# Kernel optimization log

Measured on AMD Instinct MI355X. Metric: run time of the kernel, lower is better.

The kernel has to match this reference:

```python
import jax, jax.numpy as jnp
import numpy as np

D = 32   # embedding/memory dimension
H = 2    # attention heads
DH = D // H
N_TABLE = 1_000_000
NB = 100_000      # batch nodes per type
E = 2_000_000     # edges per edge type
NE_TOT = 4_000_000
F = 32            # raw edge feature dim


def time_enc(t, w, b):
    # TimeEncode: cos(t * w + b), t: [N] -> [N, D]
    return jnp.cos(t[:, None] * w[None, :] + b[None, :])


def edge_attention_agg(h_src, h_dst, ei, ef, te, mask, Wk, Wq, Wv, n_dst):
    """One HGT-style masked multi-head attention aggregation for a single edge type.
    ei: [2, E] (src, dst local indices); ef/te: [E, D]; mask: [E] bool.
    Returns [n_dst, D] aggregated messages (segment-softmax over incoming edges)."""
    src, dst = ei[0], ei[1]
    e = src.shape[0]
    hs = h_src[src]                                   # [E, D] gather
    k = (hs @ Wk).reshape(e, H, DH)
    q = (h_dst[dst] @ Wq).reshape(e, H, DH)
    v = ((hs + ef + te) @ Wv).reshape(e, H, DH)
    s = jnp.sum(q * k, axis=-1) / jnp.sqrt(jnp.asarray(DH, h_src.dtype))  # [E, H]
    s = jnp.where(mask[:, None], s, jnp.asarray(-1e9, s.dtype))
    smax = jax.ops.segment_max(s, dst, num_segments=n_dst)                # [n_dst, H]
    p = jnp.where(mask[:, None], jnp.exp(s - smax[dst]), 0.0)
    den = jax.ops.segment_sum(p, dst, num_segments=n_dst) + 1e-9
    w = p / den[dst]                                                      # [E, H]
    return jax.ops.segment_sum((w[..., None] * v).reshape(e, D), dst, num_segments=n_dst)


def reference(memory_author, memory_paper, edge_feature,
              node_x_author, node_x_paper, ts_author, ts_paper,
              ei_writes, rel_t_writes, eidx_writes, mask_writes,
              ei_rev, rel_t_rev, eidx_rev, mask_rev,
              time_w, time_b,
              Wk_writes, Wq_writes, Wv_writes, elin_w_writes, elin_b_writes,
              Wk_rev, Wq_rev, Wv_rev, elin_w_rev, elin_b_rev,
              lin_author, lin_paper):
    # --- memory gather per node type (Mailbox.get_memory) ---
    mem_a = memory_author[node_x_author]              # [NB, D]
    mem_p = memory_paper[node_x_paper]                # [NB, D]
    # initial state = memory + node-time encoding
    h_a = mem_a + time_enc(ts_author, time_w, time_b)
    h_p = mem_p + time_enc(ts_paper, time_w, time_b)

    # --- per-edge-type feature gather + linear, and relative-time encoding ---
    mw = mask_writes != 0
    mr = mask_rev != 0
    ef_w = edge_feature[eidx_writes] @ elin_w_writes + elin_b_writes  # [E, D]
    ef_r = edge_feature[eidx_rev] @ elin_w_rev + elin_b_rev
    te_w = time_enc(rel_t_writes, time_w, time_b)
    te_r = time_enc(rel_t_rev, time_w, time_b)

    n_a, n_p = h_a.shape[0], h_p.shape[0]
    # --- 2-layer heterogeneous attention embedding ---
    for _ in range(2):
        agg_p = edge_attention_agg(h_a, h_p, ei_writes, ef_w, te_w, mw,
                                   Wk_writes, Wq_writes, Wv_writes, n_p)
        agg_a = edge_attention_agg(h_p, h_a, ei_rev, ef_r, te_r, mr,
                                   Wk_rev, Wq_rev, Wv_rev, n_a)
        h_a = jax.nn.relu(agg_a @ lin_author) + h_a
        h_p = jax.nn.relu(agg_p @ lin_paper) + h_p

    # TGN.compute_temporal_embeddings returns (node_embedding, node_memory, node_memory, node_memory)
    return (h_a, h_p, mem_a, mem_p)


def setup_inputs() -> dict:
    key = jax.random.key(0)
    ks = jax.random.split(key, 32)
    s = 1.0 / np.sqrt(D)
    inp = {
        "memory_author": jax.random.normal(ks[0], (N_TABLE, D), jnp.float32),
        "memory_paper": jax.random.normal(ks[1], (N_TABLE, D), jnp.float32),
        "edge_feature": jax.random.normal(ks[2], (NE_TOT, F), jnp.float32),
        "node_x_author": jax.random.randint(ks[3], (NB,), 0, N_TABLE, jnp.int32),
        "node_x_paper": jax.random.randint(ks[4], (NB,), 0, N_TABLE, jnp.int32),
        "ts_author": jax.random.uniform(ks[5], (NB,), jnp.float32),
        "ts_paper": jax.random.uniform(ks[6], (NB,), jnp.float32),
        "ei_writes": jax.random.randint(ks[7], (2, E), 0, NB, jnp.int32),
        "rel_t_writes": jax.random.uniform(ks[8], (E,), jnp.float32),
        "eidx_writes": jax.random.randint(ks[9], (E,), 0, NE_TOT, jnp.int32),
        "mask_writes": jax.random.randint(ks[10], (E,), 0, 3, jnp.int32),
        "ei_rev": jax.random.randint(ks[11], (2, E), 0, NB, jnp.int32),
        "rel_t_rev": jax.random.uniform(ks[12], (E,), jnp.float32),
        "eidx_rev": jax.random.randint(ks[13], (E,), 0, NE_TOT, jnp.int32),
        "mask_rev": jax.random.randint(ks[14], (E,), 0, 3, jnp.int32),
        "time_w": jax.random.normal(ks[15], (D,), jnp.float32),
        "time_b": jax.random.normal(ks[16], (D,), jnp.float32),
        "Wk_writes": jax.random.normal(ks[17], (D, D), jnp.float32) * s,
        "Wq_writes": jax.random.normal(ks[18], (D, D), jnp.float32) * s,
        "Wv_writes": jax.random.normal(ks[19], (D, D), jnp.float32) * s,
        "elin_w_writes": jax.random.normal(ks[20], (F, D), jnp.float32) * s,
        "elin_b_writes": jax.random.normal(ks[21], (D,), jnp.float32) * s,
        "Wk_rev": jax.random.normal(ks[22], (D, D), jnp.float32) * s,
        "Wq_rev": jax.random.normal(ks[23], (D, D), jnp.float32) * s,
        "Wv_rev": jax.random.normal(ks[24], (D, D), jnp.float32) * s,
        "elin_w_rev": jax.random.normal(ks[25], (F, D), jnp.float32) * s,
        "elin_b_rev": jax.random.normal(ks[26], (D,), jnp.float32) * s,
        "lin_author": jax.random.normal(ks[27], (D, D), jnp.float32) * s,
        "lin_paper": jax.random.normal(ks[28], (D, D), jnp.float32) * s,
    }
    return inp
```

## Files before the change

### kernel.cpp

```cpp
#include <hip/hip_runtime.h>
#include <hip/hip_bf16.h>


#define TPB 256

__device__ __forceinline__ unsigned int pack_bf2(float a, float b) {
    __hip_bfloat162 h2;
    h2.x = __float2bfloat16(a);
    h2.y = __float2bfloat16(b);
    return *(unsigned int*)&h2;
}

__global__ void __launch_bounds__(1024) prep_weights_kernel(
        const float* __restrict__ elin, const float* __restrict__ elinb,
        const float* __restrict__ Wv, float* __restrict__ Wc, float* __restrict__ bc) {
    int t = threadIdx.x;
    int i = t >> 5, j = t & 31;
    float acc = 0.f;
#pragma unroll
    for (int k = 0; k < 32; ++k) acc += elin[i * 32 + k] * Wv[k * 32 + j];
    Wc[i * 32 + j] = acc;
    if (i == 0) {
        float b = 0.f;
#pragma unroll
        for (int k = 0; k < 32; ++k) b += elinb[k] * Wv[k * 32 + j];
        bc[j] = b;
    }
}

__global__ void __launch_bounds__(TPB) node_init_kernel(
        const float* __restrict__ mem, const int* __restrict__ idx,
        const float* __restrict__ ts, const float* __restrict__ tw,
        const float* __restrict__ tb, float* __restrict__ h,
        float* __restrict__ out_mem, int nb) {
    int g = blockIdx.x * TPB + threadIdx.x;
    if (g >= nb * 32) return;
    int n = g >> 5, d = g & 31;
    float m = mem[(long)idx[n] * 32 + d];
    out_mem[g] = m;
    h[g] = m + __cosf(ts[n] * tw[d] + tb[d]);
}

__global__ void __launch_bounds__(TPB) hist_kernel(
        const int* __restrict__ dst, const int* __restrict__ mask,
        int* __restrict__ cnt, int e) {
    int i = blockIdx.x * TPB + threadIdx.x;
    if (i >= e) return;
    if (mask[i] != 0) atomicAdd(&cnt[dst[i]], 1);
}

__global__ void __launch_bounds__(1024) scan_kernel(
        const int* __restrict__ cnt, int* __restrict__ offs,
        int* __restrict__ cur, int nb) {
    __shared__ int s[1024];
    int t = threadIdx.x;
    int C = (nb + 1023) >> 10;
    int lo = t * C, hi = lo + C;
    if (hi > nb) hi = nb;
    if (lo > nb) lo = nb;
    int sum = 0;
    for (int i = lo; i < hi; ++i) sum += cnt[i];
    s[t] = sum;
    __syncthreads();
    for (int off = 1; off < 1024; off <<= 1) {
        int v = (t >= off) ? s[t - off] : 0;
        __syncthreads();
        s[t] += v;
        __syncthreads();
    }
    int run = s[t] - sum;
    for (int i = lo; i < hi; ++i) {
        offs[i] = run;
        cur[i] = run;
        run += cnt[i];
    }
    if (t == 1023) offs[nb] = s[1023];
}

__global__ void __launch_bounds__(TPB) scatter_kernel(
        const int* __restrict__ src, const int* __restrict__ dst,
        const int* __restrict__ mask, int* __restrict__ cur,
        int* __restrict__ csr_src, int* __restrict__ csr_eid, int e) {
    int i = blockIdx.x * TPB + threadIdx.x;
    if (i >= e) return;
    if (mask[i] != 0) {
        int p = atomicAdd(&cur[dst[i]], 1);
        csr_src[p] = src[i];
        csr_eid[p] = i;
    }
}

__global__ void __launch_bounds__(TPB) ev_kernel(
        const int* __restrict__ total_ptr, const int* __restrict__ eid,
        const int* __restrict__ eidx, const float* __restrict__ rel_t,
        const float* __restrict__ feat,
        const float* __restrict__ Wc, const float* __restrict__ bc,
        const float* __restrict__ Wv,
        const float* __restrict__ tw, const float* __restrict__ tb,
        __hip_bfloat16* __restrict__ ev) {
    int p = blockIdx.x * TPB + threadIdx.x;
    if (p >= *total_ptr) return;
    int e = eid[p];
    const float4* f4 = (const float4*)(feat + (long)eidx[e] * 32);
    float r[32];
#pragma unroll
    for (int i = 0; i < 8; ++i) {
        float4 v = f4[i];
        r[i * 4 + 0] = v.x; r[i * 4 + 1] = v.y;
        r[i * 4 + 2] = v.z; r[i * 4 + 3] = v.w;
    }
    float t = rel_t[e];
    float acc[32];
#pragma unroll
    for (int j = 0; j < 32; ++j) acc[j] = bc[j];
#pragma unroll
    for (int i = 0; i < 32; ++i) {
        float x = r[i];
#pragma unroll
        for (int j = 0; j < 32; ++j) acc[j] += x * Wc[i * 32 + j];
    }
#pragma unroll
    for (int i = 0; i < 32; ++i) {
        float x = __cosf(t * tw[i] + tb[i]);
#pragma unroll
        for (int j = 0; j < 32; ++j) acc[j] += x * Wv[i * 32 + j];
    }
    uint4* o = (uint4*)(ev + (long)p * 32);
#pragma unroll
    for (int q = 0; q < 4; ++q) {
        uint4 u;
        u.x = pack_bf2(acc[q * 8 + 0], acc[q * 8 + 1]);
        u.y = pack_bf2(acc[q * 8 + 2], acc[q * 8 + 3]);
        u.z = pack_bf2(acc[q * 8 + 4], acc[q * 8 + 5]);
        u.w = pack_bf2(acc[q * 8 + 6], acc[q * 8 + 7]);
        o[q] = u;
    }
}

__global__ void __launch_bounds__(TPB) node_mats_kernel(
        const float* __restrict__ h,
        const float* __restrict__ Wk, const float* __restrict__ Wv,
        const float* __restrict__ Wq,
        float* __restrict__ kn, float* __restrict__ hv, float* __restrict__ qn,
        int nb) {
    int n = blockIdx.x * TPB + threadIdx.x;
    if (n >= nb) return;
    const float4* h4 = (const float4*)(h + (long)n * 32);
    float r[32];
#pragma unroll
    for (int i = 0; i < 8; ++i) {
        float4 v = h4[i];
        r[i * 4 + 0] = v.x; r[i * 4 + 1] = v.y;
        r[i * 4 + 2] = v.z; r[i * 4 + 3] = v.w;
    }
    float acc[32];
#pragma unroll
    for (int j = 0; j < 32; ++j) acc[j] = 0.f;
#pragma unroll
    for (int i = 0; i < 32; ++i) {
        float x = r[i];
#pragma unroll
        for (int j = 0; j < 32; ++j) acc[j] += x * Wk[i * 32 + j];
    }
    {
        float4* o = (float4*)(kn + (long)n * 32);
#pragma unroll
        for (int q = 0; q < 8; ++q) { float4 v = {acc[q*4], acc[q*4+1], acc[q*4+2], acc[q*4+3]}; o[q] = v; }
    }
#pragma unroll
    for (int j = 0; j < 32; ++j) acc[j] = 0.f;
#pragma unroll
    for (int i = 0; i < 32; ++i) {
        float x = r[i];
#pragma unroll
        for (int j = 0; j < 32; ++j) acc[j] += x * Wv[i * 32 + j];
    }
    {
        float4* o = (float4*)(hv + (long)n * 32);
#pragma unroll
        for (int q = 0; q < 8; ++q) { float4 v = {acc[q*4], acc[q*4+1], acc[q*4+2], acc[q*4+3]}; o[q] = v; }
    }
#pragma unroll
    for (int j = 0; j < 32; ++j) acc[j] = 0.f;
#pragma unroll
    for (int i = 0; i < 32; ++i) {
        float x = r[i];
#pragma unroll
        for (int j = 0; j < 32; ++j) acc[j] += x * Wq[i * 32 + j];
    }
    {
        float4* o = (float4*)(qn + (long)n * 32);
#pragma unroll
        for (int q = 0; q < 8; ++q) { float4 v = {acc[q*4], acc[q*4+1], acc[q*4+2], acc[q*4+3]}; o[q] = v; }
    }
}

__global__ void __launch_bounds__(TPB) attn_kernel(
        const int* __restrict__ offs, const int* __restrict__ csr_src,
        const __hip_bfloat16* __restrict__ ev,
        const float* __restrict__ qn, const float* __restrict__ kn,
        const float* __restrict__ hv, float* __restrict__ agg, int nb) {
    int gid = (blockIdx.x * TPB + threadIdx.x) >> 5;
    int lane = threadIdx.x & 31;
    if (gid >= nb) return;
    float q = qn[(long)gid * 32 + lane];
    int beg = offs[gid], end = offs[gid + 1];
    float m = -1e30f, l = 0.f, acc = 0.f;
    for (int p = beg; p < end; ++p) {
        int src = csr_src[p];
        float k = kn[(long)src * 32 + lane];
        float v = hv[(long)src * 32 + lane] + __bfloat162float(ev[(long)p * 32 + lane]);
        float s = q * k;
        s += __shfl_xor(s, 1);
        s += __shfl_xor(s, 2);
        s += __shfl_xor(s, 4);
        s += __shfl_xor(s, 8);
        s *= 0.25f;
        float mn = fmaxf(m, s);
        float scale = __expf(m - mn);
        float pe = __expf(s - mn);
        l = l * scale + pe;
        acc = acc * scale + pe * v;
        m = mn;
    }
    agg[(long)gid * 32 + lane] = acc / (l + 1e-9f);
}

__global__ void __launch_bounds__(TPB) update_kernel(
        const float* __restrict__ agg, const float* __restrict__ lin,
        const float* __restrict__ h_in, float* __restrict__ h_out, int nb) {
    int n = blockIdx.x * TPB + threadIdx.x;
    if (n >= nb) return;
    const float4* a4 = (const float4*)(agg + (long)n * 32);
    float r[32];
#pragma unroll
    for (int i = 0; i < 8; ++i) {
        float4 v = a4[i];
        r[i * 4 + 0] = v.x; r[i * 4 + 1] = v.y;
        r[i * 4 + 2] = v.z; r[i * 4 + 3] = v.w;
    }
    float acc[32];
#pragma unroll
    for (int j = 0; j < 32; ++j) acc[j] = 0.f;
#pragma unroll
    for (int i = 0; i < 32; ++i) {
        float x = r[i];
#pragma unroll
        for (int j = 0; j < 32; ++j) acc[j] += x * lin[i * 32 + j];
    }
    const float4* hi4 = (const float4*)(h_in + (long)n * 32);
    float4* o = (float4*)(h_out + (long)n * 32);
#pragma unroll
    for (int q = 0; q < 8; ++q) {
        float4 hv = hi4[q];
        float4 v;
        v.x = fmaxf(acc[q * 4 + 0], 0.f) + hv.x;
        v.y = fmaxf(acc[q * 4 + 1], 0.f) + hv.y;
        v.z = fmaxf(acc[q * 4 + 2], 0.f) + hv.z;
        v.w = fmaxf(acc[q * 4 + 3], 0.f) + hv.w;
        o[q] = v;
    }
}

extern "C" void kernel_launch(void* const* d_in, const int* in_sizes, int n_in,
                              void* d_out, int out_size, void* d_ws, size_t ws_size,
                              hipStream_t stream) {
    const float* mem_a_t = (const float*)d_in[0];
    const float* mem_p_t = (const float*)d_in[1];
    const float* feat    = (const float*)d_in[2];
    const int*   nx_a    = (const int*)d_in[3];
    const int*   nx_p    = (const int*)d_in[4];
    const float* ts_a    = (const float*)d_in[5];
    const float* ts_p    = (const float*)d_in[6];
    const int*   ei_w    = (const int*)d_in[7];
    const float* rt_w    = (const float*)d_in[8];
    const int*   eidx_w  = (const int*)d_in[9];
    const int*   mask_w  = (const int*)d_in[10];
    const int*   ei_r    = (const int*)d_in[11];
    const float* rt_r    = (const float*)d_in[12];
    const int*   eidx_r  = (const int*)d_in[13];
    const int*   mask_r  = (const int*)d_in[14];
    const float* tw      = (const float*)d_in[15];
    const float* tb      = (const float*)d_in[16];
    const float* Wk_w    = (const float*)d_in[17];
    const float* Wq_w    = (const float*)d_in[18];
    const float* Wv_w    = (const float*)d_in[19];
    const float* elw_w   = (const float*)d_in[20];
    const float* elb_w   = (const float*)d_in[21];
    const float* Wk_r    = (const float*)d_in[22];
    const float* Wq_r    = (const float*)d_in[23];
    const float* Wv_r    = (const float*)d_in[24];
    const float* elw_r   = (const float*)d_in[25];
    const float* elb_r   = (const float*)d_in[26];
    const float* lin_a   = (const float*)d_in[27];
    const float* lin_p   = (const float*)d_in[28];

    const int NB = in_sizes[3];
    const int E  = in_sizes[8];

    float* out = (float*)d_out;
    float* out_ha = out;
    float* out_hp = out + (size_t)NB * 32;
    float* out_ma = out + (size_t)2 * NB * 32;
    float* out_mp = out + (size_t)3 * NB * 32;

    char* wp = (char*)d_ws;
    auto carve = [&](size_t bytes) -> void* {
        void* p = (void*)wp;
        wp += (bytes + 255) & ~(size_t)255;
        return p;
    };
    float* h_a  = (float*)carve((size_t)NB * 32 * 4);
    float* h_p  = (float*)carve((size_t)NB * 32 * 4);
    float* kn_a = (float*)carve((size_t)NB * 32 * 4);
    float* hv_a = (float*)carve((size_t)NB * 32 * 4);
    float* qn_a = (float*)carve((size_t)NB * 32 * 4);
    float* kn_p = (float*)carve((size_t)NB * 32 * 4);
    float* hv_p = (float*)carve((size_t)NB * 32 * 4);
    float* qn_p = (float*)carve((size_t)NB * 32 * 4);
    float* agg_a = (float*)carve((size_t)NB * 32 * 4);
    float* agg_p = (float*)carve((size_t)NB * 32 * 4);
    int* cnt_w  = (int*)carve((size_t)NB * 4);
    int* offs_w = (int*)carve((size_t)(NB + 1) * 4);
    int* cur_w  = (int*)carve((size_t)NB * 4);
    int* cnt_r  = (int*)carve((size_t)NB * 4);
    int* offs_r = (int*)carve((size_t)(NB + 1) * 4);
    int* cur_r  = (int*)carve((size_t)NB * 4);
    int* csr_src_w = (int*)carve((size_t)E * 4);
    int* csr_eid_w = (int*)carve((size_t)E * 4);
    int* csr_src_r = (int*)carve((size_t)E * 4);
    int* csr_eid_r = (int*)carve((size_t)E * 4);
    __hip_bfloat16* ev_w = (__hip_bfloat16*)carve((size_t)E * 32 * 2);
    __hip_bfloat16* ev_r = (__hip_bfloat16*)carve((size_t)E * 32 * 2);
    float* Wc_w = (float*)carve(1024 * 4);
    float* bc_w = (float*)carve(32 * 4);
    float* Wc_r = (float*)carve(1024 * 4);
    float* bc_r = (float*)carve(32 * 4);
    (void)ws_size; (void)n_in; (void)out_size;

    const int gE  = (E + TPB - 1) / TPB;
    const int gN32 = (NB * 32 + TPB - 1) / TPB;
    const int gN  = (NB + TPB - 1) / TPB;

    hipMemsetAsync(cnt_w, 0, (size_t)NB * 4, stream);
    hipMemsetAsync(cnt_r, 0, (size_t)NB * 4, stream);

    prep_weights_kernel<<<1, 1024, 0, stream>>>(elw_w, elb_w, Wv_w, Wc_w, bc_w);
    prep_weights_kernel<<<1, 1024, 0, stream>>>(elw_r, elb_r, Wv_r, Wc_r, bc_r);

    node_init_kernel<<<gN32, TPB, 0, stream>>>(mem_a_t, nx_a, ts_a, tw, tb, h_a, out_ma, NB);
    node_init_kernel<<<gN32, TPB, 0, stream>>>(mem_p_t, nx_p, ts_p, tw, tb, h_p, out_mp, NB);

    hist_kernel<<<gE, TPB, 0, stream>>>(ei_w + E, mask_w, cnt_w, E);
    hist_kernel<<<gE, TPB, 0, stream>>>(ei_r + E, mask_r, cnt_r, E);
    scan_kernel<<<1, 1024, 0, stream>>>(cnt_w, offs_w, cur_w, NB);
    scan_kernel<<<1, 1024, 0, stream>>>(cnt_r, offs_r, cur_r, NB);
    scatter_kernel<<<gE, TPB, 0, stream>>>(ei_w, ei_w + E, mask_w, cur_w, csr_src_w, csr_eid_w, E);
    scatter_kernel<<<gE, TPB, 0, stream>>>(ei_r, ei_r + E, mask_r, cur_r, csr_src_r, csr_eid_r, E);

    ev_kernel<<<gE, TPB, 0, stream>>>(offs_w + NB, csr_eid_w, eidx_w, rt_w, feat,
                                      Wc_w, bc_w, Wv_w, tw, tb, ev_w);
    ev_kernel<<<gE, TPB, 0, stream>>>(offs_r + NB, csr_eid_r, eidx_r, rt_r, feat,
                                      Wc_r, bc_r, Wv_r, tw, tb, ev_r);

    for (int layer = 0; layer < 2; ++layer) {
        node_mats_kernel<<<gN, TPB, 0, stream>>>(h_a, Wk_w, Wv_w, Wq_r, kn_a, hv_a, qn_a, NB);
        node_mats_kernel<<<gN, TPB, 0, stream>>>(h_p, Wk_r, Wv_r, Wq_w, kn_p, hv_p, qn_p, NB);

        attn_kernel<<<gN32, TPB, 0, stream>>>(offs_w, csr_src_w, ev_w, qn_p, kn_a, hv_a, agg_p, NB);
        attn_kernel<<<gN32, TPB, 0, stream>>>(offs_r, csr_src_r, ev_r, qn_a, kn_p, hv_p, agg_a, NB);

        if (layer == 0) {
            update_kernel<<<gN, TPB, 0, stream>>>(agg_a, lin_a, h_a, h_a, NB);
            update_kernel<<<gN, TPB, 0, stream>>>(agg_p, lin_p, h_p, h_p, NB);
        } else {
            update_kernel<<<gN, TPB, 0, stream>>>(agg_a, lin_a, h_a, out_ha, NB);
            update_kernel<<<gN, TPB, 0, stream>>>(agg_p, lin_p, h_p, out_hp, NB);
        }
    }
}
```

Measured before the change: 2.519 ms.

## Merge per-edge-type kernel pairs and pack K/V as interleaved bf16

Each pair of per-type launches (init, hist, scan, scatter, ev, node_mats, attn, update) becomes a single launch that picks its type from the block or thread index. This halves the launch count and lets both types fill the GPU together. Node K and V projections are now stored as one interleaved bf16 pair per lane, so attention does a single 4-byte gather per source instead of two fp32 gathers. The attention loop is unrolled by two. This trades K/V precision for bandwidth. node_mats writes the kv buffer twice through a strange self-referencing store, which is redundant but harmless.

```diff
diff --git a/kernel.cpp b/kernel.cpp
--- a/kernel.cpp
+++ b/kernel.cpp
@@ -4,16 +4,27 @@
 
 #define TPB 256
 
-__device__ __forceinline__ unsigned int pack_bf2(float a, float b) {
+__device__ __forceinline__ unsigned pack_bf2(float a, float b) {
     __hip_bfloat162 h2;
     h2.x = __float2bfloat16(a);
     h2.y = __float2bfloat16(b);
-    return *(unsigned int*)&h2;
-}
+    return *(unsigned*)&h2;
+}
+__device__ __forceinline__ float bflo(unsigned u) { return __uint_as_float(u << 16); }
+__device__ __forceinline__ float bfhi(unsigned u) { return __uint_as_float(u & 0xffff0000u); }
+__device__ __forceinline__ float bfu(unsigned short u) { return __uint_as_float(((unsigned)u) << 16); }
 
 __global__ void __launch_bounds__(1024) prep_weights_kernel(
-        const float* __restrict__ elin, const float* __restrict__ elinb,
-        const float* __restrict__ Wv, float* __restrict__ Wc, float* __restrict__ bc) {
+        const float* __restrict__ elw_w, const float* __restrict__ elb_w,
+        const float* __restrict__ Wv_w, float* __restrict__ Wc_w, float* __restrict__ bc_w,
+        const float* __restrict__ elw_r, const float* __restrict__ elb_r,
+        const float* __restrict__ Wv_r, float* __restrict__ Wc_r, float* __restrict__ bc_r) {
+    int ty = blockIdx.x;
+    const float* elin  = ty ? elw_r : elw_w;
+    const float* elinb = ty ? elb_r : elb_w;
+    const float* Wv    = ty ? Wv_r : Wv_w;
+    float* Wc = ty ? Wc_r : Wc_w;
+    float* bc = ty ? bc_r : bc_w;
     int t = threadIdx.x;
     int i = t >> 5, j = t & 31;
     float acc = 0.f;
@@ -29,29 +40,51 @@
 }
 
 __global__ void __launch_bounds__(TPB) node_init_kernel(
-        const float* __restrict__ mem, const int* __restrict__ idx,
-        const float* __restrict__ ts, const float* __restrict__ tw,
-        const float* __restrict__ tb, float* __restrict__ h,
-        float* __restrict__ out_mem, int nb) {
-    int g = blockIdx.x * TPB + threadIdx.x;
-    if (g >= nb * 32) return;
+        const float* __restrict__ mem_a, const int* __restrict__ idx_a,
+        const float* __restrict__ ts_a, float* __restrict__ h_a, float* __restrict__ oma,
+        const float* __restrict__ mem_p, const int* __restrict__ idx_p,
+        const float* __restrict__ ts_p, float* __restrict__ h_p, float* __restrict__ omp_,
+        const float* __restrict__ tw, const float* __restrict__ tb, int nb) {
+    int g0 = blockIdx.x * TPB + threadIdx.x;
+    int tot = nb * 32;
+    if (g0 >= 2 * tot) return;
+    int ty = g0 >= tot;
+    int g = ty ? g0 - tot : g0;
+    const float* mem = ty ? mem_p : mem_a;
+    const int* idx   = ty ? idx_p : idx_a;
+    const float* ts  = ty ? ts_p : ts_a;
+    float* h = ty ? h_p : h_a;
+    float* om = ty ? omp_ : oma;
     int n = g >> 5, d = g & 31;
     float m = mem[(long)idx[n] * 32 + d];
-    out_mem[g] = m;
+    om[g] = m;
     h[g] = m + __cosf(ts[n] * tw[d] + tb[d]);
 }
 
 __global__ void __launch_bounds__(TPB) hist_kernel(
-        const int* __restrict__ dst, const int* __restrict__ mask,
-        int* __restrict__ cnt, int e) {
-    int i = blockIdx.x * TPB + threadIdx.x;
-    if (i >= e) return;
-    if (mask[i] != 0) atomicAdd(&cnt[dst[i]], 1);
+        const int* __restrict__ dst_w, const int* __restrict__ mask_w, int* __restrict__ cnt_w,
+        const int* __restrict__ dst_r, const int* __restrict__ mask_r, int* __restrict__ cnt_r,
+        int e) {
+    int i0 = blockIdx.x * TPB + threadIdx.x;
+    if (i0 >= 2 * e) return;
+    int ty = i0 >= e;
+    int i = ty ? i0 - e : i0;
+    const int* mask = ty ? mask_r : mask_w;
+    if (mask[i] != 0) {
+        const int* dst = ty ? dst_r : dst_w;
+        int* cnt = ty ? cnt_r : cnt_w;
+        atomicAdd(&cnt[dst[i]], 1);
+    }
 }
 
 __global__ void __launch_bounds__(1024) scan_kernel(
-        const int* __restrict__ cnt, int* __restrict__ offs,
-        int* __restrict__ cur, int nb) {
+        const int* __restrict__ cnt_w, int* __restrict__ offs_w, int* __restrict__ cur_w,
+        const int* __restrict__ cnt_r, int* __restrict__ offs_r, int* __restrict__ cur_r,
+        int nb) {
+    int ty = blockIdx.x;
+    const int* cnt = ty ? cnt_r : cnt_w;
+    int* offs = ty ? offs_r : offs_w;
+    int* cur  = ty ? cur_r : cur_w;
     __shared__ int s[1024];
     int t = threadIdx.x;
     int C = (nb + 1023) >> 10;
@@ -78,28 +111,53 @@
 }
 
 __global__ void __launch_bounds__(TPB) scatter_kernel(
-        const int* __restrict__ src, const int* __restrict__ dst,
-        const int* __restrict__ mask, int* __restrict__ cur,
-        int* __restrict__ csr_src, int* __restrict__ csr_eid, int e) {
-    int i = blockIdx.x * TPB + threadIdx.x;
-    if (i >= e) return;
+        const int* __restrict__ src_w, const int* __restrict__ dst_w,
+        const int* __restrict__ mask_w, int* __restrict__ cur_w,
+        int* __restrict__ cs_w, int* __restrict__ ce_w,
+        const int* __restrict__ src_r, const int* __restrict__ dst_r,
+        const int* __restrict__ mask_r, int* __restrict__ cur_r,
+        int* __restrict__ cs_r, int* __restrict__ ce_r, int e) {
+    int i0 = blockIdx.x * TPB + threadIdx.x;
+    if (i0 >= 2 * e) return;
+    int ty = i0 >= e;
+    int i = ty ? i0 - e : i0;
+    const int* mask = ty ? mask_r : mask_w;
     if (mask[i] != 0) {
+        const int* src = ty ? src_r : src_w;
+        const int* dst = ty ? dst_r : dst_w;
+        int* cur = ty ? cur_r : cur_w;
+        int* cs = ty ? cs_w : cs_r == cs_r ? (ty ? cs_r : cs_w) : cs_w;
+        cs = ty ? cs_r : cs_w;
+        int* ce = ty ? ce_r : ce_w;
         int p = atomicAdd(&cur[dst[i]], 1);
-        csr_src[p] = src[i];
-        csr_eid[p] = i;
+        cs[p] = src[i];
+        ce[p] = i;
     }
 }
 
 __global__ void __launch_bounds__(TPB) ev_kernel(
-        const int* __restrict__ total_ptr, const int* __restrict__ eid,
-        const int* __restrict__ eidx, const float* __restrict__ rel_t,
+        int geb,
+        const int* __restrict__ tot_w, const int* __restrict__ eid_w,
+        const int* __restrict__ eidx_w, const float* __restrict__ rt_w,
+        const float* __restrict__ Wc_w, const float* __restrict__ bc_w,
+        const float* __restrict__ Wv_w, unsigned short* __restrict__ ev_w,
+        const int* __restrict__ tot_r, const int* __restrict__ eid_r,
+        const int* __restrict__ eidx_r, const float* __restrict__ rt_r,
+        const float* __restrict__ Wc_r, const float* __restrict__ bc_r,
+        const float* __restrict__ Wv_r, unsigned short* __restrict__ ev_r,
         const float* __restrict__ feat,
-        const float* __restrict__ Wc, const float* __restrict__ bc,
-        const float* __restrict__ Wv,
-        const float* __restrict__ tw, const float* __restrict__ tb,
-        __hip_bfloat16* __restrict__ ev) {
-    int p = blockIdx.x * TPB + threadIdx.x;
-    if (p >= *total_ptr) return;
+        const float* __restrict__ tw, const float* __restrict__ tb) {
+    int ty = blockIdx.x >= geb;
+    int p = (blockIdx.x - (ty ? geb : 0)) * TPB + threadIdx.x;
+    if (p >= *(ty ? tot_r : tot_w)) return;
+    const int* eid = ty ? eid_r : eid_w;
+    const int* eidx = ty ? eidx_r : eidx_w;
+    const float* rel_t = ty ? rt_r : rt_w;
+    const float* Wc = ty ? Wc_r : Wc_w;
+    const float* bc = ty ? bc_r : bc_w;
+    const float* Wv = ty ? Wv_r : Wv_w;
+    unsigned short* ev = ty ? ev_r : ev_w;
+
     int e = eid[p];
     const float4* f4 = (const float4*)(feat + (long)eidx[e] * 32);
     float r[32];
@@ -138,13 +196,24 @@
 }
 
 __global__ void __launch_bounds__(TPB) node_mats_kernel(
-        const float* __restrict__ h,
-        const float* __restrict__ Wk, const float* __restrict__ Wv,
-        const float* __restrict__ Wq,
-        float* __restrict__ kn, float* __restrict__ hv, float* __restrict__ qn,
+        const float* __restrict__ h_a, const float* __restrict__ Wk_w,
+        const float* __restrict__ Wv_w, const float* __restrict__ Wq_r,
+        unsigned* __restrict__ kv_a, float* __restrict__ qn_a,
+        const float* __restrict__ h_p, const float* __restrict__ Wk_r,
+        const float* __restrict__ Wv_r, const float* __restrict__ Wq_w,
+        unsigned* __restrict__ kv_p, float* __restrict__ qn_p,
         int nb) {
-    int n = blockIdx.x * TPB + threadIdx.x;
-    if (n >= nb) return;
+    int n0 = blockIdx.x * TPB + threadIdx.x;
+    if (n0 >= 2 * nb) return;
+    int ty = n0 >= nb;
+    int n = ty ? n0 - nb : n0;
+    const float* h  = ty ? h_p : h_a;
+    const float* Wk = ty ? Wk_r : Wk_w;
+    const float* Wv = ty ? Wv_r : Wv_w;
+    const float* Wq = ty ? Wq_w : Wq_r;
+    unsigned* kv = ty ? kv_p : kv_a;
+    float* qn = ty ? qn_p : qn_a;
+
     const float4* h4 = (const float4*)(h + (long)n * 32);
     float r[32];
 #pragma unroll
@@ -153,84 +222,132 @@
         r[i * 4 + 0] = v.x; r[i * 4 + 1] = v.y;
         r[i * 4 + 2] = v.z; r[i * 4 + 3] = v.w;
     }
-    float acc[32];
-#pragma unroll
-    for (int j = 0; j < 32; ++j) acc[j] = 0.f;
+    float ak[32], av[32], aq[32];
+#pragma unroll
+    for (int j = 0; j < 32; ++j) { ak[j] = 0.f; av[j] = 0.f; aq[j] = 0.f; }
 #pragma unroll
     for (int i = 0; i < 32; ++i) {
         float x = r[i];
 #pragma unroll
-        for (int j = 0; j < 32; ++j) acc[j] += x * Wk[i * 32 + j];
+        for (int j = 0; j < 32; ++j) {
+            ak[j] += x * Wk[i * 32 + j];
+            av[j] += x * Wv[i * 32 + j];
+            aq[j] += x * Wq[i * 32 + j];
+        }
+    }
+    uint4* ko = (uint4*)(kv + (long)n * 32);
+#pragma unroll
+    for (int q = 0; q < 8; ++q) {
+        uint4 u;
+        u.x = pack_bf2(ak[q * 4 + 0], av[q * 4 + 0]);
+        u.y = pack_bf2(ak[q * 4 + 1], av[q * 4 + 1]);
+        u.z = pack_bf2(ak[q * 4 + 2], av[q * 4 + 2]);
+        u.w = pack_bf2(ak[q * 4 + 3], av[q * 4 + 3]);
+        ko[q >> 1] = (q & 1) ? ko[q >> 1] : u;
     }
     {
-        float4* o = (float4*)(kn + (long)n * 32);
-#pragma unroll
-        for (int q = 0; q < 8; ++q) { float4 v = {acc[q*4], acc[q*4+1], acc[q*4+2], acc[q*4+3]}; o[q] = v; }
-    }
-#pragma unroll
-    for (int j = 0; j < 32; ++j) acc[j] = 0.f;
-#pragma unroll
-    for (int i = 0; i < 32; ++i) {
-        float x = r[i];
-#pragma unroll
-        for (int j = 0; j < 32; ++j) acc[j] += x * Wv[i * 32 + j];
-    }
-    {
-        float4* o = (float4*)(hv + (long)n * 32);
-#pragma unroll
-        for (int q = 0; q < 8; ++q) { float4 v = {acc[q*4], acc[q*4+1], acc[q*4+2], acc[q*4+3]}; o[q] = v; }
-    }
-#pragma unroll
-    for (int j = 0; j < 32; ++j) acc[j] = 0.f;
-#pragma unroll
-    for (int i = 0; i < 32; ++i) {
-        float x = r[i];
-#pragma unroll
-        for (int j = 0; j < 32; ++j) acc[j] += x * Wq[i * 32 + j];
-    }
-    {
-        float4* o = (float4*)(qn + (long)n * 32);
-#pragma unroll
-        for (int q = 0; q < 8; ++q) { float4 v = {acc[q*4], acc[q*4+1], acc[q*4+2], acc[q*4+3]}; o[q] = v; }
+        uint4* o = (uint4*)(kv + (long)n * 32);
+#pragma unroll
+        for (int q = 0; q < 8; ++q) {
+            uint4 u;
+            u.x = pack_bf2(ak[q * 4 + 0], av[q * 4 + 0]);
+            u.y = pack_bf2(ak[q * 4 + 1], av[q * 4 + 1]);
+            u.z = pack_bf2(ak[q * 4 + 2], av[q * 4 + 2]);
+            u.w = pack_bf2(ak[q * 4 + 3], av[q * 4 + 3]);
+            o[q] = u;
+        }
+    }
+    float4* qo = (float4*)(qn + (long)n * 32);
+#pragma unroll
+    for (int q = 0; q < 8; ++q) {
+        float4 v = {aq[q * 4 + 0], aq[q * 4 + 1], aq[q * 4 + 2], aq[q * 4 + 3]};
+        qo[q] = v;
     }
 }
 
 __global__ void __launch_bounds__(TPB) attn_kernel(
-        const int* __restrict__ offs, const int* __restrict__ csr_src,
-        const __hip_bfloat16* __restrict__ ev,
-        const float* __restrict__ qn, const float* __restrict__ kn,
-        const float* __restrict__ hv, float* __restrict__ agg, int nb) {
-    int gid = (blockIdx.x * TPB + threadIdx.x) >> 5;
+        const int* __restrict__ offs_w, const int* __restrict__ src_w,
+        const unsigned short* __restrict__ ev_w, const float* __restrict__ qn_p,
+        const unsigned* __restrict__ kv_a, float* __restrict__ agg_p,
+        const int* __restrict__ offs_r, const int* __restrict__ src_r,
+        const unsigned short* __restrict__ ev_r, const float* __restrict__ qn_a,
+        const unsigned* __restrict__ kv_p, float* __restrict__ agg_a, int nb) {
+    int g = (blockIdx.x * TPB + threadIdx.x) >> 5;
     int lane = threadIdx.x & 31;
-    if (gid >= nb) return;
-    float q = qn[(long)gid * 32 + lane];
-    int beg = offs[gid], end = offs[gid + 1];
+    if (g >= 2 * nb) return;
+    int dir = g >= nb;
+    int node = dir ? g - nb : g;
+    const int* offs = dir ? offs_r : offs_w;
+    const int* srcs = dir ? src_r : src_w;
+    const unsigned short* ev = dir ? ev_r : ev_w;
+    const float* qn = dir ? qn_a : qn_p;
+    const unsigned* kv = dir ? kv_p : kv_a;
+    float* agg = dir ? agg_a : agg_p;
+
+    float q = qn[(long)node * 32 + lane];
+    int beg = offs[node], end = offs[node + 1];
     float m = -1e30f, l = 0.f, acc = 0.f;
-    for (int p = beg; p < end; ++p) {
-        int src = csr_src[p];
-        float k = kn[(long)src * 32 + lane];
-        float v = hv[(long)src * 32 + lane] + __bfloat162float(ev[(long)p * 32 + lane]);
-        float s = q * k;
-        s += __shfl_xor(s, 1);
-        s += __shfl_xor(s, 2);
-        s += __shfl_xor(s, 4);
-        s += __shfl_xor(s, 8);
+    int p = beg;
+    for (; p + 2 <= end; p += 2) {
+        int s0 = srcs[p], s1 = srcs[p + 1];
+        unsigned u0 = kv[(long)s0 * 32 + lane];
+        unsigned u1 = kv[(long)s1 * 32 + lane];
+        float e0 = bfu(ev[(long)p * 32 + lane]);
+        float e1 = bfu(ev[(long)(p + 1) * 32 + lane]);
+        {
+            float s = q * bflo(u0);
+            s += __shfl_xor(s, 1); s += __shfl_xor(s, 2);
+            s += __shfl_xor(s, 4); s += __shfl_xor(s, 8);
+            s *= 0.25f;
+            float mn = fmaxf(m, s);
+            float sc = __expf(m - mn), pe = __expf(s - mn);
+            l = l * sc + pe;
+            acc = acc * sc + pe * (bfhi(u0) + e0);
+            m = mn;
+        }
+        {
+            float s = q * bflo(u1);
+            s += __shfl_xor(s, 1); s += __shfl_xor(s, 2);
+            s += __shfl_xor(s, 4); s += __shfl_xor(s, 8);
+            s *= 0.25f;
+            float mn = fmaxf(m, s);
+            float sc = __expf(m - mn), pe = __expf(s - mn);
+            l = l * sc + pe;
+            acc = acc * sc + pe * (bfhi(u1) + e1);
+            m = mn;
+        }
+    }
+    if (p < end) {
+        int s0 = srcs[p];
+        unsigned u0 = kv[(long)s0 * 32 + lane];
+        float e0 = bfu(ev[(long)p * 32 + lane]);
+        float s = q * bflo(u0);
+        s += __shfl_xor(s, 1); s += __shfl_xor(s, 2);
+        s += __shfl_xor(s, 4); s += __shfl_xor(s, 8);
         s *= 0.25f;
         float mn = fmaxf(m, s);
-        float scale = __expf(m - mn);
-        float pe = __expf(s - mn);
-        l = l * scale + pe;
-        acc = acc * scale + pe * v;
+        float sc = __expf(m - mn), pe = __expf(s - mn);
+        l = l * sc + pe;
+        acc = acc * sc + pe * (bfhi(u0) + e0);
         m = mn;
     }
-    agg[(long)gid * 32 + lane] = acc / (l + 1e-9f);
+    agg[(long)node * 32 + lane] = acc / (l + 1e-9f);
 }
 
 __global__ void __launch_bounds__(TPB) update_kernel(
-        const float* __restrict__ agg, const float* __restrict__ lin,
-        const float* __restrict__ h_in, float* __restrict__ h_out, int nb) {
-    int n = blockIdx.x * TPB + threadIdx.x;
-    if (n >= nb) return;
+        const float* __restrict__ agg_a, const float* __restrict__ lin_a,
+        const float* __restrict__ h_a, float* __restrict__ ho_a,
+        const float* __restrict__ agg_p, const float* __restrict__ lin_p,
+        const float* __restrict__ h_p, float* __restrict__ ho_p, int nb) {
+    int n0 = blockIdx.x * TPB + threadIdx.x;
+    if (n0 >= 2 * nb) return;
+    int ty = n0 >= nb;
+    int n = ty ? n0 - nb : n0;
+    const float* agg = ty ? agg_p : agg_a;
+    const float* lin = ty ? lin_p : lin_a;
+    const float* h_in = ty ? h_p : h_a;
+    float* h_out = ty ? ho_p : ho_a;
+
     const float4* a4 = (const float4*)(agg + (long)n * 32);
     float r[32];
 #pragma unroll
@@ -312,70 +429,72 @@
     };
     float* h_a  = (float*)carve((size_t)NB * 32 * 4);
     float* h_p  = (float*)carve((size_t)NB * 32 * 4);
-    float* kn_a = (float*)carve((size_t)NB * 32 * 4);
-    float* hv_a = (float*)carve((size_t)NB * 32 * 4);
+    unsigned* kv_a = (unsigned*)carve((size_t)NB * 32 * 4);
+    unsigned* kv_p = (unsigned*)carve((size_t)NB * 32 * 4);
     float* qn_a = (float*)carve((size_t)NB * 32 * 4);
-    float* kn_p = (float*)carve((size_t)NB * 32 * 4);
-    float* hv_p = (float*)carve((size_t)NB * 32 * 4);
     float* qn_p = (float*)carve((size_t)NB * 32 * 4);
     float* agg_a = (float*)carve((size_t)NB * 32 * 4);
     float* agg_p = (float*)carve((size_t)NB * 32 * 4);
     int* cnt_w  = (int*)carve((size_t)NB * 4);
+    int* cnt_r  = (int*)carve((size_t)NB * 4);
     int* offs_w = (int*)carve((size_t)(NB + 1) * 4);
     int* cur_w  = (int*)carve((size_t)NB * 4);
-    int* cnt_r  = (int*)carve((size_t)NB * 4);
     int* offs_r = (int*)carve((size_t)(NB + 1) * 4);
     int* cur_r  = (int*)carve((size_t)NB * 4);
     int* csr_src_w = (int*)carve((size_t)E * 4);
     int* csr_eid_w = (int*)carve((size_t)E * 4);
     int* csr_src_r = (int*)carve((size_t)E * 4);
     int* csr_eid_r = (int*)carve((size_t)E * 4);
-    __hip_bfloat16* ev_w = (__hip_bfloat16*)carve((size_t)E * 32 * 2);
-    __hip_bfloat16* ev_r = (__hip_bfloat16*)carve((size_t)E * 32 * 2);
+    unsigned short* ev_w = (unsigned short*)carve((size_t)E * 32 * 2);
+    unsigned short* ev_r = (unsigned short*)carve((size_t)E * 32 * 2);
     float* Wc_w = (float*)carve(1024 * 4);
     float* bc_w = (float*)carve(32 * 4);
     float* Wc_r = (float*)carve(1024 * 4);
     float* bc_r = (float*)carve(32 * 4);
     (void)ws_size; (void)n_in; (void)out_size;
 
-    const int gE  = (E + TPB - 1) / TPB;
-    const int gN32 = (NB * 32 + TPB - 1) / TPB;
-    const int gN  = (NB + TPB - 1) / TPB;
-
-    hipMemsetAsync(cnt_w, 0, (size_t)NB * 4, stream);
-    hipMemsetAsync(cnt_r, 0, (size_t)NB * 4, stream);
-
-    prep_weights_kernel<<<1, 1024, 0, stream>>>(elw_w, elb_w, Wv_w, Wc_w, bc_w);
-    prep_weights_kernel<<<1, 1024, 0, stream>>>(elw_r, elb_r, Wv_r, Wc_r, bc_r);
-
-    node_init_kernel<<<gN32, TPB, 0, stream>>>(mem_a_t, nx_a, ts_a, tw, tb, h_a, out_ma, NB);
-    node_init_kernel<<<gN32, TPB, 0, stream>>>(mem_p_t, nx_p, ts_p, tw, tb, h_p, out_mp, NB);
-
-    hist_kernel<<<gE, TPB, 0, stream>>>(ei_w + E, mask_w, cnt_w, E);
-    hist_kernel<<<gE, TPB, 0, stream>>>(ei_r + E, mask_r, cnt_r, E);
-    scan_kernel<<<1, 1024, 0, stream>>>(cnt_w, offs_w, cur_w, NB);
-    scan_kernel<<<1, 1024, 0, stream>>>(cnt_r, offs_r, cur_r, NB);
-    scatter_kernel<<<gE, TPB, 0, stream>>>(ei_w, ei_w + E, mask_w, cur_w, csr_src_w, csr_eid_w, E);
-    scatter_kernel<<<gE, TPB, 0, stream>>>(ei_r, ei_r + E, mask_r, cur_r, csr_src_r, csr_eid_r, E);
-
-    ev_kernel<<<gE, TPB, 0, stream>>>(offs_w + NB, csr_eid_w, eidx_w, rt_w, feat,
-                                      Wc_w, bc_w, Wv_w, tw, tb, ev_w);
-    ev_kernel<<<gE, TPB, 0, stream>>>(offs_r + NB, csr_eid_r, eidx_r, rt_r, feat,
-                                      Wc_r, bc_r, Wv_r, tw, tb, ev_r);
+    const int gE2  = (2 * E + TPB - 1) / TPB;
+    const int geb  = (E + TPB - 1) / TPB;
+    const int gN64 = (2 * NB * 32 + TPB - 1) / TPB;
+    const int gN2  = (2 * NB + TPB - 1) / TPB;
+
+    {
+        size_t pad = ((size_t)NB * 4 + 255) & ~(size_t)255;
+        hipMemsetAsync(cnt_w, 0, pad + (size_t)NB * 4, stream);
+    }
+
+    prep_weights_kernel<<<2, 1024, 0, stream>>>(elw_w, elb_w, Wv_w, Wc_w, bc_w,
+                                                elw_r, elb_r, Wv_r, Wc_r, bc_r);
+    node_init_kernel<<<gN64, TPB, 0, stream>>>(mem_a_t, nx_a, ts_a, h_a, out_ma,
+                                               mem_p_t, nx_p, ts_p, h_p, out_mp,
+                                               tw, tb, NB);
+
+    hist_kernel<<<gE2, TPB, 0, stream>>>(ei_w + E, mask_w, cnt_w,
+                                         ei_r + E, mask_r, cnt_r, E);
+    scan_kernel<<<2, 1024, 0, stream>>>(cnt_w, offs_w, cur_w, cnt_r, offs_r, cur_r, NB);
+    scatter_kernel<<<gE2, TPB, 0, stream>>>(ei_w, ei_w + E, mask_w, cur_w, csr_src_w, csr_eid_w,
+                                            ei_r, ei_r + E, mask_r, cur_r, csr_src_r, csr_eid_r, E);
+
+    ev_kernel<<<2 * geb, TPB, 0, stream>>>(geb,
+            offs_w + NB, csr_eid_w, eidx_w, rt_w, Wc_w, bc_w, Wv_w, ev_w,
+            offs_r + NB, csr_eid_r, eidx_r, rt_r, Wc_r, bc_r, Wv_r, ev_r,
+            feat, tw, tb);
 
     for (int layer = 0; layer < 2; ++layer) {
-        node_mats_kernel<<<gN, TPB, 0, stream>>>(h_a, Wk_w, Wv_w, Wq_r, kn_a, hv_a, qn_a, NB);
-        node_mats_kernel<<<gN, TPB, 0, stream>>>(h_p, Wk_r, Wv_r, Wq_w, kn_p, hv_p, qn_p, NB);
-
-        attn_kernel<<<gN32, TPB, 0, stream>>>(offs_w, csr_src_w, ev_w, qn_p, kn_a, hv_a, agg_p, NB);
-        attn_kernel<<<gN32, TPB, 0, stream>>>(offs_r, csr_src_r, ev_r, qn_a, kn_p, hv_p, agg_a, NB);
+        node_mats_kernel<<<gN2, TPB, 0, stream>>>(
+                h_a, Wk_w, Wv_w, Wq_r, kv_a, qn_a,
+                h_p, Wk_r, Wv_r, Wq_w, kv_p, qn_p, NB);
+
+        attn_kernel<<<2 * ((NB * 32 + TPB - 1) / TPB), TPB, 0, stream>>>(
+                offs_w, csr_src_w, ev_w, qn_p, kv_a, agg_p,
+                offs_r, csr_src_r, ev_r, qn_a, kv_p, agg_a, NB);
 
         if (layer == 0) {
-            update_kernel<<<gN, TPB, 0, stream>>>(agg_a, lin_a, h_a, h_a, NB);
-            update_kernel<<<gN, TPB, 0, stream>>>(agg_p, lin_p, h_p, h_p, NB);
+            update_kernel<<<gN2, TPB, 0, stream>>>(agg_a, lin_a, h_a, h_a,
+                                                   agg_p, lin_p, h_p, h_p, NB);
         } else {
-            update_kernel<<<gN, TPB, 0, stream>>>(agg_a, lin_a, h_a, out_ha, NB);
-            update_kernel<<<gN, TPB, 0, stream>>>(agg_p, lin_p, h_p, out_hp, NB);
+            update_kernel<<<gN2, TPB, 0, stream>>>(agg_a, lin_a, h_a, out_ha,
+                                                   agg_p, lin_p, h_p, out_hp, NB);
         }
     }
 }
```

Result: faster. 2.268 ms (-10.0%).
